# Kernel tuning notes

Hardware: AMD Instinct MI355X
Metric: run time of the kernel (lower is better)

Reference implementation:

```python
import jax, jax.numpy as jnp
import numpy as np

B, IN_DIM, OUT_DIM, N_KNOTS = 8192, 1024, 1024, 4


def setup_inputs() -> dict:
    key = jax.random.key(0)
    k_feat, k_phase, k_w = jax.random.split(key, 3)
    feats = jax.random.normal(k_feat, (B, IN_DIM), dtype=jnp.float32)
    phase = jax.random.uniform(k_phase, (B, 1), dtype=jnp.float32)  # phase in [0,1)
    x = jnp.concatenate([feats, phase], axis=1)  # [B, IN_DIM+1]
    bound = np.sqrt(6.0 / (OUT_DIM * IN_DIM))
    weight_knots = jax.random.uniform(
        k_w, (N_KNOTS, OUT_DIM, IN_DIM), dtype=jnp.float32, minval=-bound, maxval=bound)
    bias_knots = jnp.zeros((N_KNOTS, OUT_DIM), dtype=jnp.float32)
    return {"x": x, "weight_knots": weight_knots, "bias_knots": bias_knots}


def _cubic(y, mu):
    # Catmull-Rom cubic blend over the 4 gathered knots, y: [B,4,D], mu: [B,1]
    y0, y1, y2, y3 = y[:, 0], y[:, 1], y[:, 2], y[:, 3]
    return ((-0.5 * y0 + 1.5 * y1 - 1.5 * y2 + 0.5 * y3) * mu * mu * mu
            + (y0 - 2.5 * y1 + 2.0 * y2 - 0.5 * y3) * mu * mu
            + (-0.5 * y0 + 0.5 * y2) * mu + y1)


def reference(x, weight_knots, bias_knots):
    K = weight_knots.shape[0]
    phase = x[:, -1]            # [B]
    feats = x[:, :-1]           # [B, IN_DIM]
    pscale = K * phase
    mu = jnp.mod(pscale, 1.0)[:, None]                       # [B, 1]
    i1 = jnp.mod(pscale.astype(jnp.int32), K)
    idx = jnp.stack([jnp.mod(i1 - 1, K), i1,
                     jnp.mod(i1 + 1, K), jnp.mod(i1 + 2, K)], axis=1)  # [B, 4]
    # Exploit linearity: matvec against each knot matrix once, then blend.
    # Mathematically identical to cubic(W0,..,W3) @ feats + cubic(b0,..,b3).
    yk = jnp.einsum('koi,bi->bko', weight_knots, feats)      # [B, K, OUT]
    y4 = jnp.take_along_axis(yk, idx[:, :, None], axis=1)    # [B, 4, OUT]
    b4 = bias_knots[idx]                                     # [B, 4, OUT]
    res = _cubic(y4 + b4, mu)                                # cubic is linear in y
    return jax.nn.elu(res)
```

## Files before the change

kernel.cpp:

```cpp
#include <hip/hip_runtime.h>
#include <math.h>

#define IN_DIM 1024
#define OUT_DIM 1024
#define NROWS 8192
#define XSTRIDE 1025

typedef __attribute__((ext_vector_type(8))) short bf16x8;
typedef __attribute__((ext_vector_type(4))) float f32x4;

static __device__ __forceinline__ unsigned f2bf(float f) {
  union { float f; unsigned u; } v; v.f = f;
  unsigned u = v.u;
  return (u + 0x7fffu + ((u >> 16) & 1u)) >> 16;
}

__global__ __launch_bounds__(256) void prep_kernel(
    const float* __restrict__ x, const float* __restrict__ W,
    unsigned short* __restrict__ Wb, unsigned short* __restrict__ F,
    float* __restrict__ coef)
{
  const int blk = blockIdx.x;
  if (blk < 2048) {
    const int t = blk * 256 + threadIdx.x;
    const int flat = t * 8;
    const int k = flat >> 20;
    const int o = (flat >> 10) & 1023;
    const int i = flat & 1023;
    const float4 fa = *reinterpret_cast<const float4*>(W + flat);
    const float4 fb = *reinterpret_cast<const float4*>(W + flat + 4);
    uint4 pk;
    pk.x = f2bf(fa.x) | (f2bf(fa.y) << 16);
    pk.y = f2bf(fa.z) | (f2bf(fa.w) << 16);
    pk.z = f2bf(fb.x) | (f2bf(fb.y) << 16);
    pk.w = f2bf(fb.z) | (f2bf(fb.w) << 16);
    const int g = (o & 15) | (k << 4) | ((o >> 4) << 6);
    *reinterpret_cast<uint4*>(Wb + (size_t)g * 1024 + i) = pk;
  } else {
    const int b = blk - 2048;
    const float* xr = x + (size_t)b * XSTRIDE;
    const int i = threadIdx.x * 4;
    ushort4 vv;
    vv.x = (unsigned short)f2bf(xr[i]);     vv.y = (unsigned short)f2bf(xr[i + 1]);
    vv.z = (unsigned short)f2bf(xr[i + 2]); vv.w = (unsigned short)f2bf(xr[i + 3]);
    *reinterpret_cast<ushort4*>(F + (size_t)b * 1024 + i) = vv;
    if (threadIdx.x == 0) {
      const float ps = 4.0f * xr[IN_DIM];
      const int ip = (int)ps;
      const int i1 = ip & 3;
      const float mu = ps - (float)ip;
      const float mu2 = mu * mu, mu3 = mu2 * mu;
      const float c0 = -0.5f * mu3 +        mu2 - 0.5f * mu;
      const float c1 =  1.5f * mu3 - 2.5f * mu2 + 1.0f;
      const float c2 = -1.5f * mu3 + 2.0f * mu2 + 0.5f * mu;
      const float c3 =  0.5f * mu3 - 0.5f * mu2;
      const int d0 = (0-i1)&3, d1 = (1-i1)&3, d2 = (2-i1)&3, d3 = (3-i1)&3;
      float4 cv;
      cv.x = d0==0 ? c1 : d0==1 ? c2 : d0==2 ? c3 : c0;
      cv.y = d1==0 ? c1 : d1==1 ? c2 : d1==2 ? c3 : c0;
      cv.z = d2==0 ? c1 : d2==1 ? c2 : d2==2 ? c3 : c0;
      cv.w = d3==0 ? c1 : d3==1 ? c2 : d3==2 ? c3 : c0;
      *reinterpret_cast<float4*>(coef + (size_t)b * 4) = cv;
    }
  }
}

#define BM 128
#define BN 128
#define BK 64

__global__ __launch_bounds__(256, 4) void gemm_kernel(
    const unsigned short* __restrict__ F,
    const unsigned short* __restrict__ Wb,
    const float* __restrict__ coef,
    const float* __restrict__ bias,
    float* __restrict__ out)
{
  __shared__ unsigned short As[BM * BK];
  __shared__ unsigned short Bs[BN * BK];

  const int lin = blockIdx.y * 32 + blockIdx.x;
  const int xcd = lin & 7;
  const int idx = lin >> 3;
  const int bx  = (xcd & 1) * 16 + (idx & 15);
  const int by  = (xcd >> 1) * 16 + (idx >> 4);

  const int tid  = threadIdx.x;
  const int wave = tid >> 6;
  const int lane = tid & 63;
  const int row0  = by * BM;
  const int col0g = bx * BN;

  const int srow = tid >> 3;
  const int scc  = tid & 7;
  const int sgc  = (scc ^ (srow & 7)) * 8;

  const int wr = (wave >> 1) * 64;
  const int wc = (wave & 1) * 64;
  const int fm = lane & 15;
  const int fq = lane >> 4;

  f32x4 acc[4][4];
  const f32x4 zero = {0.f, 0.f, 0.f, 0.f};
  #pragma unroll
  for (int a = 0; a < 4; a++)
    #pragma unroll
    for (int b = 0; b < 4; b++)
      acc[a][b] = zero;

  const unsigned short* Abase = F  + (size_t)row0  * 1024;
  const unsigned short* Bbase = Wb + (size_t)col0g * 1024;

  for (int kb = 0; kb < 1024; kb += BK) {
    #pragma unroll
    for (int it = 0; it < 4; it++) {
      const int r = srow + it * 32;
      __builtin_amdgcn_global_load_lds(
          (const __attribute__((address_space(1))) void*)(Abase + (size_t)r * 1024 + kb + sgc),
          (__attribute__((address_space(3))) void*)(As + r * BK + scc * 8), 16, 0, 0);
      __builtin_amdgcn_global_load_lds(
          (const __attribute__((address_space(1))) void*)(Bbase + (size_t)r * 1024 + kb + sgc),
          (__attribute__((address_space(3))) void*)(Bs + r * BK + scc * 8), 16, 0, 0);
    }
    __syncthreads();

    #pragma unroll
    for (int kk = 0; kk < BK; kk += 32) {
      bf16x8 af[4], bfr[4];
      #pragma unroll
      for (int mi = 0; mi < 4; mi++) {
        const int r  = wr + mi * 16 + fm;
        const int lc = ((kk >> 3) + fq) ^ (fm & 7);
        af[mi] = *reinterpret_cast<const bf16x8*>(As + r * BK + lc * 8);
      }
      #pragma unroll
      for (int ni = 0; ni < 4; ni++) {
        const int r  = wc + ni * 16 + fm;
        const int lc = ((kk >> 3) + fq) ^ (fm & 7);
        bfr[ni] = *reinterpret_cast<const bf16x8*>(Bs + r * BK + lc * 8);
      }
      #pragma unroll
      for (int mi = 0; mi < 4; mi++)
        #pragma unroll
        for (int ni = 0; ni < 4; ni++)
          acc[mi][ni] = __builtin_amdgcn_mfma_f32_16x16x32_bf16(
              af[mi], bfr[ni], acc[mi][ni], 0, 0, 0);
    }
    __syncthreads();
  }

  const int o = fm + 16 * (2 * bx + (wave & 1));
  const float b0 = bias[o];
  const float b1 = bias[OUT_DIM + o];
  const float b2 = bias[2 * OUT_DIM + o];
  const float b3 = bias[3 * OUT_DIM + o];
  #pragma unroll
  for (int mi = 0; mi < 4; mi++) {
    #pragma unroll
    for (int r = 0; r < 4; r++) {
      const int rloc = wr + mi * 16 + (fq << 2) + r;
      const float4 c = *reinterpret_cast<const float4*>(coef + (size_t)(row0 + rloc) * 4);
      float v = c.x * (acc[mi][0][r] + b0)
              + c.y * (acc[mi][1][r] + b1)
              + c.z * (acc[mi][2][r] + b2)
              + c.w * (acc[mi][3][r] + b3);
      const float e = __expf(v) - 1.0f;
      v = (v > 0.0f) ? v : e;
      out[(size_t)(row0 + rloc) * OUT_DIM + o] = v;
    }
  }
}

extern "C" void kernel_launch(void* const* d_in, const int* in_sizes, int n_in,
                              void* d_out, int out_size, void* d_ws, size_t ws_size,
                              hipStream_t stream) {
  const float* x  = (const float*)d_in[0];
  const float* wk = (const float*)d_in[1];
  const float* bk = (const float*)d_in[2];
  float* out = (float*)d_out;

  char* ws = (char*)d_ws;
  unsigned short* Wb = (unsigned short*)ws;
  unsigned short* F  = (unsigned short*)(ws + (8u << 20));
  float* coef        = (float*)(ws + (24u << 20));

  hipLaunchKernelGGL(prep_kernel, dim3(2048 + NROWS), dim3(256), 0, stream,
                     x, wk, Wb, F, coef);
  hipLaunchKernelGGL(gemm_kernel, dim3(4096 / BN, NROWS / BM), dim3(256), 0, stream,
                     F, Wb, coef, bk, out);
}
```

Before: 160.1 us.

## Double-buffer LDS tiles with BK=32 to overlap global loads with MFMA

Result: slower. 169.4 us (+5.8%).

```diff
diff --git a/kernel.cpp b/kernel.cpp
--- a/kernel.cpp
+++ b/kernel.cpp
@@ -67,7 +67,7 @@
 
 #define BM 128
 #define BN 128
-#define BK 64
+#define BK 32
 
 __global__ __launch_bounds__(256, 4) void gemm_kernel(
     const unsigned short* __restrict__ F,
@@ -76,8 +76,8 @@
     const float* __restrict__ bias,
     float* __restrict__ out)
 {
-  __shared__ unsigned short As[BM * BK];
-  __shared__ unsigned short Bs[BN * BK];
+  __shared__ unsigned short As[2][BM * BK];
+  __shared__ unsigned short Bs[2][BN * BK];
 
   const int lin = blockIdx.y * 32 + blockIdx.x;
   const int xcd = lin & 7;
@@ -91,14 +91,15 @@
   const int row0  = by * BM;
   const int col0g = bx * BN;
 
-  const int srow = tid >> 3;
-  const int scc  = tid & 7;
-  const int sgc  = (scc ^ (srow & 7)) * 8;
+  const int srow = tid >> 2;
+  const int scc  = tid & 3;
+  const int sgc  = (scc ^ ((srow >> 1) & 3)) * 8;
 
   const int wr = (wave >> 1) * 64;
   const int wc = (wave & 1) * 64;
   const int fm = lane & 15;
   const int fq = lane >> 4;
+  const int lc = (fq ^ ((fm >> 1) & 3)) * 8;
 
   f32x4 acc[4][4];
   const f32x4 zero = {0.f, 0.f, 0.f, 0.f};
@@ -111,43 +112,49 @@
   const unsigned short* Abase = F  + (size_t)row0  * 1024;
   const unsigned short* Bbase = Wb + (size_t)col0g * 1024;
 
-  for (int kb = 0; kb < 1024; kb += BK) {
+#define STG(p, kb) do {                                                        \
+    _Pragma("unroll")                                                          \
+    for (int it_ = 0; it_ < 2; ++it_) {                                        \
+      const int r_ = srow + it_ * 64;                                          \
+      __builtin_amdgcn_global_load_lds(                                        \
+        (const __attribute__((address_space(1))) void*)(                       \
+            Abase + (size_t)r_ * 1024 + (kb) + sgc),                           \
+        (__attribute__((address_space(3))) void*)(&As[p][r_ * BK + scc * 8]),  \
+        16, 0, 0);                                                             \
+      __builtin_amdgcn_global_load_lds(                                        \
+        (const __attribute__((address_space(1))) void*)(                       \
+            Bbase + (size_t)r_ * 1024 + (kb) + sgc),                           \
+        (__attribute__((address_space(3))) void*)(&Bs[p][r_ * BK + scc * 8]),  \
+        16, 0, 0);                                                             \
+    } } while (0)
+
+  STG(0, 0);
+  asm volatile("s_waitcnt vmcnt(0)" ::: "memory");
+  __builtin_amdgcn_s_barrier();
+
+  #pragma unroll 1
+  for (int t = 0; t < 32; ++t) {
+    const int p = t & 1;
+    if (t < 31) STG(p ^ 1, (t + 1) * BK);
+
+    bf16x8 af[4], bfr[4];
     #pragma unroll
-    for (int it = 0; it < 4; it++) {
-      const int r = srow + it * 32;
-      __builtin_amdgcn_global_load_lds(
-          (const __attribute__((address_space(1))) void*)(Abase + (size_t)r * 1024 + kb + sgc),
-          (__attribute__((address_space(3))) void*)(As + r * BK + scc * 8), 16, 0, 0);
-      __builtin_amdgcn_global_load_lds(
-          (const __attribute__((address_space(1))) void*)(Bbase + (size_t)r * 1024 + kb + sgc),
-          (__attribute__((address_space(3))) void*)(Bs + r * BK + scc * 8), 16, 0, 0);
-    }
-    __syncthreads();
+    for (int mi = 0; mi < 4; mi++)
+      af[mi] = *reinterpret_cast<const bf16x8*>(&As[p][(wr + mi * 16 + fm) * BK + lc]);
+    #pragma unroll
+    for (int ni = 0; ni < 4; ni++)
+      bfr[ni] = *reinterpret_cast<const bf16x8*>(&Bs[p][(wc + ni * 16 + fm) * BK + lc]);
+    #pragma unroll
+    for (int mi = 0; mi < 4; mi++)
+      #pragma unroll
+      for (int ni = 0; ni < 4; ni++)
+        acc[mi][ni] = __builtin_amdgcn_mfma_f32_16x16x32_bf16(
+            af[mi], bfr[ni], acc[mi][ni], 0, 0, 0);
 
-    #pragma unroll
-    for (int kk = 0; kk < BK; kk += 32) {
-      bf16x8 af[4], bfr[4];
-      #pragma unroll
-      for (int mi = 0; mi < 4; mi++) {
-        const int r  = wr + mi * 16 + fm;
-        const int lc = ((kk >> 3) + fq) ^ (fm & 7);
-        af[mi] = *reinterpret_cast<const bf16x8*>(As + r * BK + lc * 8);
-      }
-      #pragma unroll
-      for (int ni = 0; ni < 4; ni++) {
-        const int r  = wc + ni * 16 + fm;
-        const int lc = ((kk >> 3) + fq) ^ (fm & 7);
-        bfr[ni] = *reinterpret_cast<const bf16x8*>(Bs + r * BK + lc * 8);
-      }
-      #pragma unroll
-      for (int mi = 0; mi < 4; mi++)
-        #pragma unroll
-        for (int ni = 0; ni < 4; ni++)
-          acc[mi][ni] = __builtin_amdgcn_mfma_f32_16x16x32_bf16(
-              af[mi], bfr[ni], acc[mi][ni], 0, 0, 0);
-    }
-    __syncthreads();
+    asm volatile("s_waitcnt vmcnt(0)" ::: "memory");
+    __builtin_amdgcn_s_barrier();
   }
+#undef STG
 
   const int o = fm + 16 * (2 * bx + (wave & 1));
   const float b0 = bias[o];
```
